# Optimization experiments

Hardware: AMD Instinct MI355X
Metric: run time of the kernel (lower is better)

## Reference

```python
import jax, jax.numpy as jnp
import numpy as np

N_HEADS = 16

def rotate_half(x):
    x1, x2 = jnp.split(x, 2, axis=-1)
    return jnp.concatenate([-x2, x1], axis=-1)

def setup_inputs() -> dict:
    key = jax.random.key(0)
    ks = jax.random.split(key, 6)
    dim = 2048
    B, T = 4, 2048
    x = jax.random.normal(ks[0], (B, T, dim), dtype=jnp.float32)
    pos = jnp.arange(T, dtype=jnp.float32).reshape(T, 1, 1)
    def w(k):
        return jax.random.normal(k, (dim, dim), dtype=jnp.float32) * 0.02
    return {
        "x": x, "pos": pos,
        "wq_w": w(ks[1]), "wq_b": jnp.zeros((dim,), jnp.float32),
        "wk_w": w(ks[2]), "wk_b": jnp.zeros((dim,), jnp.float32),
        "wv_w": w(ks[3]), "wv_b": jnp.zeros((dim,), jnp.float32),
        "wo_w": w(ks[4]), "wo_b": jnp.zeros((dim,), jnp.float32),
    }

def reference(x, pos, wq_w, wq_b, wk_w, wk_b, wv_w, wv_b, wo_w, wo_b):
    B, T, dim = x.shape
    H = N_HEADS
    hd = dim // H
    q = (x @ wq_w.T + wq_b).reshape(B, T, H, hd)
    k = (x @ wk_w.T + wk_b).reshape(B, T, H, hd)
    v = (x @ wv_w.T + wv_b).reshape(B, T, H, hd)
    # RoPE: freq over half the head dim, sin/cos tiled to full head dim
    freq = 1.0 / (10000.0 ** (jnp.arange(0, hd, 2, dtype=jnp.float32) / hd))  # [hd/2]
    ang = pos * freq                      # [T,1,hd/2]
    sin = jnp.concatenate([jnp.sin(ang), jnp.sin(ang)], axis=-1)  # [T,1,hd]
    cos = jnp.concatenate([jnp.cos(ang), jnp.cos(ang)], axis=-1)  # [T,1,hd]
    q = q * cos + rotate_half(q) * sin
    k = k * cos + rotate_half(k) * sin
    # [B,H,T,hd]
    q = q.transpose(0, 2, 1, 3)
    k = k.transpose(0, 2, 1, 3)
    v = v.transpose(0, 2, 1, 3)
    scale = 1.0 / np.sqrt(hd).astype(np.float32)
    attn = jnp.einsum('bhqd,bhkd->bhqk', q, k) * scale  # [B,H,T,T]
    attn = jax.nn.softmax(attn, axis=-1)
    out = jnp.einsum('bhqk,bhkd->bhqd', attn, v)        # [B,H,T,hd]
    out = out.transpose(0, 2, 1, 3).reshape(B, T, dim)
    return out @ wo_w.T + wo_b
```

## Files before the change

### kernel.cpp

```cpp
#include <hip/hip_runtime.h>


using floatx4  = __attribute__((ext_vector_type(4))) float;
using short8   = __attribute__((ext_vector_type(8))) short;
using ushortx4 = __attribute__((ext_vector_type(4))) unsigned short;

#define DEVFN static __device__ __forceinline__

DEVFN unsigned short f2bf(float f) {
  unsigned u = __builtin_bit_cast(unsigned, f);
  u += 0x7fffu + ((u >> 16) & 1u);
  return (unsigned short)(u >> 16);
}
DEVFN float bf2f(unsigned short h) {
  return __builtin_bit_cast(float, ((unsigned)h) << 16);
}

DEVFN void async_cp16(const unsigned short* g, unsigned short* l) {
  __builtin_amdgcn_global_load_lds(
      (const __attribute__((address_space(1))) void*)g,
      (__attribute__((address_space(3))) void*)l,
      16, 0, 0);
}

__global__ __launch_bounds__(256) void cast_kernel(const float4* __restrict__ in,
                                                   ushortx4* __restrict__ out) {
  long u = (long)blockIdx.x * 256 + threadIdx.x;
  float4 v = in[u];
  out[u] = (ushortx4){f2bf(v.x), f2bf(v.y), f2bf(v.z), f2bf(v.w)};
}

__global__ __launch_bounds__(256) void rope_kernel(unsigned short* __restrict__ Q,
                                                   unsigned short* __restrict__ K,
                                                   const float* __restrict__ pos) {
  long idx = (long)blockIdx.x * 256 + threadIdx.x;
  unsigned short* arr = (idx >> 23) ? K : Q;
  long rem = idx & ((1L << 23) - 1);
  long row = rem >> 6;
  int j = (int)(rem & 63);
  int t = (int)(row & 2047);
  float ang = pos[t] * exp2f(-0.20762051f * (float)j);
  float s = sinf(ang), c = cosf(ang);
  unsigned short* base = arr + (row << 7);
  float x1 = bf2f(base[j]), x2 = bf2f(base[j + 64]);
  base[j]      = f2bf(x1 * c - x2 * s);
  base[j + 64] = f2bf(x2 * c + x1 * s);
}

template <int MODE>
__global__ __launch_bounds__(256) void gemm_bt(const unsigned short* __restrict__ A,
                                               const unsigned short* __restrict__ Bw,
                                               const float* __restrict__ bias,
                                               void* __restrict__ Cout) {
  constexpr int K = 2048;
  __shared__ __align__(16) unsigned short lds_a[128 * 64];
  __shared__ __align__(16) unsigned short lds_b[128 * 64];
  const int tid = threadIdx.x;
  const int wave = tid >> 6, lane = tid & 63;
  const int ln15 = lane & 15, quad = lane >> 4;
  const int wr = wave >> 1, wc = wave & 1;
  const int bid = blockIdx.x;
  const int xcd = bid & 7, sl = bid >> 3;
  const int m0 = (xcd * 8 + (sl & 7)) * 128;
  const int n0 = (sl >> 3) * 128;

  floatx4 acc[4][4];
#pragma unroll
  for (int i = 0; i < 4; ++i)
#pragma unroll
    for (int j = 0; j < 4; ++j) acc[i][j] = (floatx4){0.f, 0.f, 0.f, 0.f};

  for (int k0 = 0; k0 < K; k0 += 64) {
    __syncthreads();
#pragma unroll
    for (int j = 0; j < 4; ++j) {
      int u = j * 256 + tid;
      int row = u >> 3;
      int c = (u & 7) ^ (row & 7);
      async_cp16(A + (long)(m0 + row) * K + (k0 + c * 8),
                 lds_a + (j * 256 + wave * 64) * 8);
    }
#pragma unroll
    for (int j = 0; j < 4; ++j) {
      int u = j * 256 + tid;
      int row = u >> 3;
      int c = (u & 7) ^ (row & 7);
      async_cp16(Bw + (long)(n0 + row) * K + (k0 + c * 8),
                 lds_b + (j * 256 + wave * 64) * 8);
    }
    asm volatile("s_waitcnt vmcnt(0)" ::: "memory");
    __syncthreads();
#pragma unroll
    for (int ks = 0; ks < 2; ++ks) {
      short8 af[4], bf[4];
#pragma unroll
      for (int mi = 0; mi < 4; ++mi) {
        int row = wr * 64 + mi * 16 + ln15;
        int phys = (ks * 4 + quad) ^ (row & 7);
        af[mi] = *(const short8*)(lds_a + row * 64 + phys * 8);
      }
#pragma unroll
      for (int ni = 0; ni < 4; ++ni) {
        int row = wc * 64 + ni * 16 + ln15;
        int phys = (ks * 4 + quad) ^ (row & 7);
        bf[ni] = *(const short8*)(lds_b + row * 64 + phys * 8);
      }
#pragma unroll
      for (int mi = 0; mi < 4; ++mi)
#pragma unroll
        for (int ni = 0; ni < 4; ++ni)
          acc[mi][ni] = __builtin_amdgcn_mfma_f32_16x16x32_bf16(af[mi], bf[ni],
                                                                acc[mi][ni], 0, 0, 0);
    }
  }

#pragma unroll
  for (int mi = 0; mi < 4; ++mi) {
#pragma unroll
    for (int ni = 0; ni < 4; ++ni) {
      int n = n0 + wc * 64 + ni * 16 + ln15;
      float bv = bias[n];
      int mbase = m0 + wr * 64 + mi * 16 + quad * 4;
      if (MODE == 0) {
        int h = n >> 7, d = n & 127;
#pragma unroll
        for (int r = 0; r < 4; ++r) {
          int m = mbase + r;
          int b = m >> 11, t = m & 2047;
          ((unsigned short*)Cout)[((((long)(b * 16 + h)) << 11) + t) * 128 + d] =
              f2bf(acc[mi][ni][r] + bv);
        }
      } else if (MODE == 1) {
        int h = n >> 7, d = n & 127;
        int b = mbase >> 11, t = mbase & 2047;
        ushortx4 v;
#pragma unroll
        for (int r = 0; r < 4; ++r) v[r] = f2bf(acc[mi][ni][r] + bv);
        *(ushortx4*)((unsigned short*)Cout +
                     ((((long)(b * 16 + h)) << 7) + d) * 2048 + t) = v;
      } else {
#pragma unroll
        for (int r = 0; r < 4; ++r) {
          int m = mbase + r;
          ((float*)Cout)[(long)m * 2048 + n] = acc[mi][ni][r] + bv;
        }
      }
    }
  }
}

__global__ __launch_bounds__(512, 2) void flash_kernel(
    const unsigned short* __restrict__ Q,
    const unsigned short* __restrict__ Kmat,
    const unsigned short* __restrict__ Vt,
    unsigned short* __restrict__ Out) {
  constexpr int T = 2048;
  constexpr float SCALE = 0.08838834764831845f;
  __shared__ __align__(16) unsigned short lds[49152];

  const int tid = threadIdx.x;
  const int wave = tid >> 6, lane = tid & 63;
  const int ln15 = lane & 15, quad = lane >> 4;
  const int l7 = ln15 & 7;
  const int bid = blockIdx.x;
  const int xcd = bid & 7, sl = bid >> 3;
  const int bh = xcd * 8 + (sl >> 3);
  const int q0 = (sl & 7) * 256;

  const unsigned short* Qb = Q + (long)bh * T * 128;
  const unsigned short* Kb = Kmat + (long)bh * T * 128;
  const unsigned short* Vb = Vt + (long)bh * 128 * T;
  unsigned short* pw = lds + 32768 + wave * 2048;

  short8 qf[2][4];
#pragma unroll
  for (int mi = 0; mi < 2; ++mi)
#pragma unroll
    for (int ks = 0; ks < 4; ++ks)
      qf[mi][ks] = *(const short8*)(Qb + (long)(q0 + wave * 32 + mi * 16 + ln15) * 128 +
                                    ks * 32 + quad * 8);

#define STAGE_KV(t, kdst, vdst)                                                  \
  do {                                                                           \
    _Pragma("unroll") for (int j = 0; j < 2; ++j) {                              \
      int u = j * 512 + tid;                                                     \
      int row = u >> 4;                                                          \
      int c = (u & 15) ^ (row & 15);                                             \
      async_cp16(Kb + (long)((t) * 64 + row) * 128 + c * 8,                      \
                 (kdst) + (j * 512 + wave * 64) * 8);                            \
    }                                                                            \
    _Pragma("unroll") for (int j = 0; j < 2; ++j) {                              \
      int u = j * 512 + tid;                                                     \
      int row = u >> 3;                                                          \
      int c = (u & 7) ^ (row & 7);                                               \
      async_cp16(Vb + (long)row * T + (t) * 64 + c * 8,                          \
                 (vdst) + (j * 512 + wave * 64) * 8);                            \
    }                                                                            \
  } while (0)

  STAGE_KV(0, lds, lds + 16384);
  asm volatile("s_waitcnt vmcnt(0)" ::: "memory");
  __syncthreads();

  floatx4 oacc[2][8];
#pragma unroll
  for (int mi = 0; mi < 2; ++mi)
#pragma unroll
    for (int nj = 0; nj < 8; ++nj) oacc[mi][nj] = (floatx4){0.f, 0.f, 0.f, 0.f};
  float mst[2][4], lsp[2][4];
#pragma unroll
  for (int mi = 0; mi < 2; ++mi)
#pragma unroll
    for (int r = 0; r < 4; ++r) { mst[mi][r] = -1e30f; lsp[mi][r] = 0.f; }

  for (int t = 0; t < 32; ++t) {
    unsigned short* kc = lds + (t & 1) * 8192;
    unsigned short* vc = lds + 16384 + (t & 1) * 8192;
    if (t < 31) {
      unsigned short* kn = lds + ((t + 1) & 1) * 8192;
      unsigned short* vn = lds + 16384 + ((t + 1) & 1) * 8192;
      STAGE_KV(t + 1, kn, vn);
    }

    floatx4 sacc[2][4];
#pragma unroll
    for (int mi = 0; mi < 2; ++mi)
#pragma unroll
      for (int ni = 0; ni < 4; ++ni) sacc[mi][ni] = (floatx4){0.f, 0.f, 0.f, 0.f};
#pragma unroll
    for (int ks = 0; ks < 4; ++ks) {
      short8 bfr[4];
#pragma unroll
      for (int ni = 0; ni < 4; ++ni) {
        int row = ni * 16 + ln15;
        int phys = (ks * 4 + quad) ^ ln15;
        bfr[ni] = *(const short8*)(kc + row * 128 + phys * 8);
      }
      __builtin_amdgcn_s_setprio(1);
#pragma unroll
      for (int mi = 0; mi < 2; ++mi)
#pragma unroll
        for (int ni = 0; ni < 4; ++ni)
          sacc[mi][ni] = __builtin_amdgcn_mfma_f32_16x16x32_bf16(qf[mi][ks], bfr[ni],
                                                                 sacc[mi][ni], 0, 0, 0);
      __builtin_amdgcn_s_setprio(0);
    }

#pragma unroll
    for (int mi = 0; mi < 2; ++mi)
#pragma unroll
      for (int r = 0; r < 4; ++r) {
        float mx = fmaxf(fmaxf(sacc[mi][0][r], sacc[mi][1][r]),
                         fmaxf(sacc[mi][2][r], sacc[mi][3][r]));
#pragma unroll
        for (int off = 1; off < 16; off <<= 1) mx = fmaxf(mx, __shfl_xor(mx, off, 16));
        mx *= SCALE;
        float mold = mst[mi][r];
        float mnew = fmaxf(mold, mx);
        float alpha = __expf(mold - mnew);
        float rs = 0.f;
#pragma unroll
        for (int ni = 0; ni < 4; ++ni) {
          float p = __expf(sacc[mi][ni][r] * SCALE - mnew);
          sacc[mi][ni][r] = p;
          rs += p;
        }
        mst[mi][r] = mnew;
        lsp[mi][r] = lsp[mi][r] * alpha + rs;
#pragma unroll
        for (int nj = 0; nj < 8; ++nj) oacc[mi][nj][r] *= alpha;
      }

#pragma unroll
    for (int mi = 0; mi < 2; ++mi)
#pragma unroll
      for (int ni = 0; ni < 4; ++ni) {
        int cc = ni * 2 + (ln15 >> 3);
#pragma unroll
        for (int r = 0; r < 4; ++r) {
          int m = mi * 16 + quad * 4 + r;
          pw[m * 64 + (cc ^ (m & 7)) * 8 + l7] = f2bf(sacc[mi][ni][r]);
        }
      }

#pragma unroll
    for (int ks = 0; ks < 2; ++ks) {
      short8 af[2], bv[8];
#pragma unroll
      for (int mi = 0; mi < 2; ++mi) {
        int phys = (ks * 4 + quad) ^ l7;
        af[mi] = *(const short8*)(pw + (mi * 16 + ln15) * 64 + phys * 8);
      }
#pragma unroll
      for (int nj = 0; nj < 8; ++nj) {
        int row = nj * 16 + ln15;
        int phys = (ks * 4 + quad) ^ (row & 7);
        bv[nj] = *(const short8*)(vc + row * 64 + phys * 8);
      }
      __builtin_amdgcn_s_setprio(1);
#pragma unroll
      for (int mi = 0; mi < 2; ++mi)
#pragma unroll
        for (int nj = 0; nj < 8; ++nj)
          oacc[mi][nj] = __builtin_amdgcn_mfma_f32_16x16x32_bf16(af[mi], bv[nj],
                                                                 oacc[mi][nj], 0, 0, 0);
      __builtin_amdgcn_s_setprio(0);
    }

    asm volatile("s_waitcnt vmcnt(0)" ::: "memory");
    __syncthreads();
  }
#undef STAGE_KV

  float rinv[2][4];
#pragma unroll
  for (int mi = 0; mi < 2; ++mi)
#pragma unroll
    for (int r = 0; r < 4; ++r) {
      float l = lsp[mi][r];
#pragma unroll
      for (int off = 1; off < 16; off <<= 1) l += __shfl_xor(l, off, 16);
      rinv[mi][r] = 1.f / l;
    }
#pragma unroll
  for (int mi = 0; mi < 2; ++mi)
#pragma unroll
    for (int nj = 0; nj < 8; ++nj)
#pragma unroll
      for (int r = 0; r < 4; ++r)
        lds[(wave * 32 + mi * 16 + quad * 4 + r) * 128 + nj * 16 + ln15] =
            f2bf(oacc[mi][nj][r] * rinv[mi][r]);
  __syncthreads();
  const int b = bh >> 4, h = bh & 15;
  long obase = ((long)(b * T + q0) << 11) + h * 128;
#pragma unroll
  for (int j = 0; j < 8; ++j) {
    int u = j * 512 + tid;
    int r = u >> 4, c = u & 15;
    *(short8*)(Out + obase + ((long)r << 11) + c * 8) =
        *(const short8*)(lds + r * 128 + c * 8);
  }
}

extern "C" void kernel_launch(void* const* d_in, const int* in_sizes, int n_in,
                              void* d_out, int out_size, void* d_ws, size_t ws_size,
                              hipStream_t stream) {
  const float* x    = (const float*)d_in[0];
  const float* pos  = (const float*)d_in[1];
  const float* wq_w = (const float*)d_in[2];
  const float* wq_b = (const float*)d_in[3];
  const float* wk_w = (const float*)d_in[4];
  const float* wk_b = (const float*)d_in[5];
  const float* wv_w = (const float*)d_in[6];
  const float* wv_b = (const float*)d_in[7];
  const float* wo_w = (const float*)d_in[8];
  const float* wo_b = (const float*)d_in[9];

  unsigned short* xb  = (unsigned short*)d_ws;
  unsigned short* wqb = xb  + (1u << 24);
  unsigned short* wkb = wqb + (1u << 22);
  unsigned short* wvb = wkb + (1u << 22);
  unsigned short* wob = wvb + (1u << 22);
  unsigned short* qb  = wob + (1u << 22);
  unsigned short* kb  = qb  + (1u << 24);
  unsigned short* vtb = kb  + (1u << 24);
  unsigned short* ab  = vtb + (1u << 24);

  cast_kernel<<<16384, 256, 0, stream>>>((const float4*)x, (ushortx4*)xb);
  cast_kernel<<<4096, 256, 0, stream>>>((const float4*)wq_w, (ushortx4*)wqb);
  cast_kernel<<<4096, 256, 0, stream>>>((const float4*)wk_w, (ushortx4*)wkb);
  cast_kernel<<<4096, 256, 0, stream>>>((const float4*)wv_w, (ushortx4*)wvb);
  cast_kernel<<<4096, 256, 0, stream>>>((const float4*)wo_w, (ushortx4*)wob);

  gemm_bt<0><<<1024, 256, 0, stream>>>(xb, wqb, wq_b, (void*)qb);
  gemm_bt<0><<<1024, 256, 0, stream>>>(xb, wkb, wk_b, (void*)kb);
  gemm_bt<1><<<1024, 256, 0, stream>>>(xb, wvb, wv_b, (void*)vtb);
  rope_kernel<<<65536, 256, 0, stream>>>(qb, kb, pos);
  flash_kernel<<<512, 512, 0, stream>>>(qb, kb, vtb, ab);
  gemm_bt<2><<<1024, 256, 0, stream>>>(ab, wob, wo_b, d_out);
}
```

Before: 748.4 us.

## Rewrite projection GEMM with 256x256 tiles, triple-buffered async loads, LDS-staged epilogue

Rewrites the projection GEMM to use 256x256 block tiles with 8 waves and a K-step of 32. Global-to-LDS copies are triple-buffered so loads for step t+2 overlap MFMA work on step t, replacing the load-wait-compute loop with a barrier every iteration. Output is staged through swizzled LDS so global stores become 16-byte coalesced writes, including the transposed V layout. The trade-off is more registers for the 8x4 accumulators and only 256 blocks, which may leave some CUs idle on a 256-CU part.

```diff
diff --git a/kernel.cpp b/kernel.cpp
--- a/kernel.cpp
+++ b/kernel.cpp
@@ -48,102 +48,208 @@
 }
 
 template <int MODE>
-__global__ __launch_bounds__(256) void gemm_bt(const unsigned short* __restrict__ A,
-                                               const unsigned short* __restrict__ Bw,
-                                               const float* __restrict__ bias,
-                                               void* __restrict__ Cout) {
+__global__ __launch_bounds__(512, 2) void gemm_bt(const unsigned short* __restrict__ A,
+                                                  const unsigned short* __restrict__ Bw,
+                                                  const float* __restrict__ bias,
+                                                  void* __restrict__ Cout) {
   constexpr int K = 2048;
-  __shared__ __align__(16) unsigned short lds_a[128 * 64];
-  __shared__ __align__(16) unsigned short lds_b[128 * 64];
+  constexpr int NT = 64;
+  __shared__ __align__(16) unsigned short lds[49152];
   const int tid = threadIdx.x;
   const int wave = tid >> 6, lane = tid & 63;
   const int ln15 = lane & 15, quad = lane >> 4;
-  const int wr = wave >> 1, wc = wave & 1;
+  const int wm = wave >> 2, wn = wave & 3;
   const int bid = blockIdx.x;
   const int xcd = bid & 7, sl = bid >> 3;
-  const int m0 = (xcd * 8 + (sl & 7)) * 128;
-  const int n0 = (sl >> 3) * 128;
-
-  floatx4 acc[4][4];
-#pragma unroll
-  for (int i = 0; i < 4; ++i)
+  const int m0 = (xcd * 4 + (sl & 3)) * 256;
+  const int n0 = (sl >> 2) * 256;
+
+  const unsigned short* srcA0;
+  const unsigned short* srcA1;
+  const unsigned short* srcB0;
+  const unsigned short* srcB1;
+  {
+    int u = tid;
+    int L = u >> 3, cc = (u & 7) ^ (L & 7);
+    int row = L * 2 + (cc >> 2), col = (cc & 3) * 8;
+    srcA0 = A + (long)(m0 + row) * K + col;
+    srcB0 = Bw + (long)(n0 + row) * K + col;
+  }
+  {
+    int u = tid + 512;
+    int L = u >> 3, cc = (u & 7) ^ (L & 7);
+    int row = L * 2 + (cc >> 2), col = (cc & 3) * 8;
+    srcA1 = A + (long)(m0 + row) * K + col;
+    srcB1 = Bw + (long)(n0 + row) * K + col;
+  }
+  const int sdst = wave * 512;
+
+#define STAGE_G(t, bufp)                                                \
+  do {                                                                  \
+    async_cp16(srcA0 + (long)(t) * 32, (bufp) + sdst);                  \
+    async_cp16(srcA1 + (long)(t) * 32, (bufp) + 4096 + sdst);           \
+    async_cp16(srcB0 + (long)(t) * 32, (bufp) + 8192 + sdst);           \
+    async_cp16(srcB1 + (long)(t) * 32, (bufp) + 12288 + sdst);          \
+  } while (0)
+
+  int offA[8], offB[4];
+#pragma unroll
+  for (int mi = 0; mi < 8; ++mi) {
+    int row = wm * 128 + mi * 16 + ln15;
+    int line = row >> 1, cc = (row & 1) * 4 + quad;
+    offA[mi] = line * 64 + (cc ^ (line & 7)) * 8;
+  }
+#pragma unroll
+  for (int nj = 0; nj < 4; ++nj) {
+    int row = wn * 64 + nj * 16 + ln15;
+    int line = row >> 1, cc = (row & 1) * 4 + quad;
+    offB[nj] = 8192 + line * 64 + (cc ^ (line & 7)) * 8;
+  }
+
+  floatx4 acc[8][4];
+#pragma unroll
+  for (int i = 0; i < 8; ++i)
 #pragma unroll
     for (int j = 0; j < 4; ++j) acc[i][j] = (floatx4){0.f, 0.f, 0.f, 0.f};
 
-  for (int k0 = 0; k0 < K; k0 += 64) {
-    __syncthreads();
-#pragma unroll
-    for (int j = 0; j < 4; ++j) {
-      int u = j * 256 + tid;
-      int row = u >> 3;
-      int c = (u & 7) ^ (row & 7);
-      async_cp16(A + (long)(m0 + row) * K + (k0 + c * 8),
-                 lds_a + (j * 256 + wave * 64) * 8);
-    }
-#pragma unroll
-    for (int j = 0; j < 4; ++j) {
-      int u = j * 256 + tid;
-      int row = u >> 3;
-      int c = (u & 7) ^ (row & 7);
-      async_cp16(Bw + (long)(n0 + row) * K + (k0 + c * 8),
-                 lds_b + (j * 256 + wave * 64) * 8);
-    }
-    asm volatile("s_waitcnt vmcnt(0)" ::: "memory");
-    __syncthreads();
-#pragma unroll
-    for (int ks = 0; ks < 2; ++ks) {
-      short8 af[4], bf[4];
-#pragma unroll
-      for (int mi = 0; mi < 4; ++mi) {
-        int row = wr * 64 + mi * 16 + ln15;
-        int phys = (ks * 4 + quad) ^ (row & 7);
-        af[mi] = *(const short8*)(lds_a + row * 64 + phys * 8);
-      }
-#pragma unroll
-      for (int ni = 0; ni < 4; ++ni) {
-        int row = wc * 64 + ni * 16 + ln15;
-        int phys = (ks * 4 + quad) ^ (row & 7);
-        bf[ni] = *(const short8*)(lds_b + row * 64 + phys * 8);
-      }
-#pragma unroll
-      for (int mi = 0; mi < 4; ++mi)
-#pragma unroll
-        for (int ni = 0; ni < 4; ++ni)
-          acc[mi][ni] = __builtin_amdgcn_mfma_f32_16x16x32_bf16(af[mi], bf[ni],
-                                                                acc[mi][ni], 0, 0, 0);
-    }
-  }
-
-#pragma unroll
-  for (int mi = 0; mi < 4; ++mi) {
-#pragma unroll
-    for (int ni = 0; ni < 4; ++ni) {
-      int n = n0 + wc * 64 + ni * 16 + ln15;
-      float bv = bias[n];
-      int mbase = m0 + wr * 64 + mi * 16 + quad * 4;
-      if (MODE == 0) {
-        int h = n >> 7, d = n & 127;
-#pragma unroll
-        for (int r = 0; r < 4; ++r) {
-          int m = mbase + r;
-          int b = m >> 11, t = m & 2047;
-          ((unsigned short*)Cout)[((((long)(b * 16 + h)) << 11) + t) * 128 + d] =
-              f2bf(acc[mi][ni][r] + bv);
+  unsigned short* const bA0 = lds;
+  unsigned short* const bA1 = lds + 16384;
+  unsigned short* const bA2 = lds + 32768;
+
+  STAGE_G(0, bA0);
+  STAGE_G(1, bA1);
+  asm volatile("s_waitcnt vmcnt(4)" ::: "memory");
+  __builtin_amdgcn_s_barrier();
+
+  int cb = 0;
+  for (int t = 0; t < NT; ++t) {
+    unsigned short* cur = (cb == 0) ? bA0 : ((cb == 1) ? bA1 : bA2);
+    if (t < NT - 2) {
+      int nb = cb ? cb - 1 : 2;
+      unsigned short* nxt = (nb == 0) ? bA0 : ((nb == 1) ? bA1 : bA2);
+      STAGE_G(t + 2, nxt);
+    }
+    short8 af[8], bf4[4];
+#pragma unroll
+    for (int mi = 0; mi < 8; ++mi) af[mi] = *(const short8*)(cur + offA[mi]);
+#pragma unroll
+    for (int nj = 0; nj < 4; ++nj) bf4[nj] = *(const short8*)(cur + offB[nj]);
+    __builtin_amdgcn_s_setprio(1);
+#pragma unroll
+    for (int mi = 0; mi < 8; ++mi)
+#pragma unroll
+      for (int nj = 0; nj < 4; ++nj)
+        acc[mi][nj] = __builtin_amdgcn_mfma_f32_16x16x32_bf16(af[mi], bf4[nj],
+                                                              acc[mi][nj], 0, 0, 0);
+    __builtin_amdgcn_s_setprio(0);
+    if (t < NT - 2) {
+      asm volatile("s_waitcnt vmcnt(4)" ::: "memory");
+    } else if (t == NT - 2) {
+      asm volatile("s_waitcnt vmcnt(0)" ::: "memory");
+    }
+    __builtin_amdgcn_s_barrier();
+    cb = (cb == 2) ? 0 : cb + 1;
+  }
+#undef STAGE_G
+
+  const int b_ = m0 >> 11;
+  const int t0m = m0 & 2047;
+  const int h0 = n0 >> 7;
+
+  if (MODE == 0) {
+#pragma unroll
+    for (int rnd = 0; rnd < 2; ++rnd) {
+      __syncthreads();
+      if (wm == rnd) {
+#pragma unroll
+        for (int nj = 0; nj < 4; ++nj) {
+          int nloc = wn * 64 + nj * 16 + ln15;
+          float bv = bias[n0 + nloc];
+#pragma unroll
+          for (int mi = 0; mi < 8; ++mi)
+#pragma unroll
+            for (int r = 0; r < 4; ++r) {
+              int tl = mi * 16 + quad * 4 + r;
+              int phys = (nloc >> 3) ^ (tl & 15);
+              lds[tl * 256 + phys * 8 + (nloc & 7)] = f2bf(acc[mi][nj][r] + bv);
+            }
         }
-      } else if (MODE == 1) {
-        int h = n >> 7, d = n & 127;
-        int b = mbase >> 11, t = mbase & 2047;
-        ushortx4 v;
-#pragma unroll
-        for (int r = 0; r < 4; ++r) v[r] = f2bf(acc[mi][ni][r] + bv);
-        *(ushortx4*)((unsigned short*)Cout +
-                     ((((long)(b * 16 + h)) << 7) + d) * 2048 + t) = v;
-      } else {
-#pragma unroll
-        for (int r = 0; r < 4; ++r) {
-          int m = mbase + r;
-          ((float*)Cout)[(long)m * 2048 + n] = acc[mi][ni][r] + bv;
+      }
+      __syncthreads();
+#pragma unroll
+      for (int j = 0; j < 8; ++j) {
+        int u = j * 512 + tid;
+        int tl = u >> 5, c = u & 31;
+        int phys = c ^ (tl & 15);
+        int h = h0 + (c >> 4);
+        int tt = t0m + rnd * 128 + tl;
+        *(short8*)((unsigned short*)Cout +
+                   ((((long)(b_ * 16 + h)) << 11) + tt) * 128 + (c & 15) * 8) =
+            *(const short8*)(lds + tl * 256 + phys * 8);
+      }
+    }
+  } else if (MODE == 1) {
+#pragma unroll
+    for (int rnd = 0; rnd < 2; ++rnd) {
+      __syncthreads();
+      if (wm == rnd) {
+#pragma unroll
+        for (int nj = 0; nj < 4; ++nj) {
+          int nloc = wn * 64 + nj * 16 + ln15;
+          float bv = bias[n0 + nloc];
+#pragma unroll
+          for (int mi = 0; mi < 8; ++mi)
+#pragma unroll
+            for (int r = 0; r < 4; ++r) {
+              int tl = mi * 16 + quad * 4 + r;
+              int phys = (tl >> 3) ^ (nloc & 15);
+              lds[nloc * 128 + phys * 8 + (tl & 7)] = f2bf(acc[mi][nj][r] + bv);
+            }
         }
+      }
+      __syncthreads();
+#pragma unroll
+      for (int j = 0; j < 8; ++j) {
+        int u = j * 512 + tid;
+        int nloc = u >> 4, c = u & 15;
+        int phys = c ^ (nloc & 15);
+        int h = h0 + (nloc >> 7), d = nloc & 127;
+        *(short8*)((unsigned short*)Cout +
+                   ((((long)(b_ * 16 + h)) << 7) + d) * 2048 + t0m + rnd * 128 + c * 8) =
+            *(const short8*)(lds + nloc * 128 + phys * 8);
+      }
+    }
+  } else {
+    float* lf = (float*)lds;
+#pragma unroll
+    for (int rnd = 0; rnd < 4; ++rnd) {
+      __syncthreads();
+      if (wm == (rnd >> 1)) {
+#pragma unroll
+        for (int nj = 0; nj < 4; ++nj) {
+          int nloc = wn * 64 + nj * 16 + ln15;
+          float bv = bias[n0 + nloc];
+#pragma unroll
+          for (int mh = 0; mh < 4; ++mh) {
+            int mi = (rnd & 1) * 4 + mh;
+#pragma unroll
+            for (int r = 0; r < 4; ++r) {
+              int tl = mh * 16 + quad * 4 + r;
+              int phys = (nloc >> 2) ^ (tl & 15);
+              lf[tl * 256 + phys * 4 + (nloc & 3)] = acc[mi][nj][r] + bv;
+            }
+          }
+        }
+      }
+      __syncthreads();
+#pragma unroll
+      for (int j = 0; j < 8; ++j) {
+        int u = j * 512 + tid;
+        int tl = u >> 6, c = u & 63;
+        int phys = c ^ (tl & 15);
+        int m = m0 + rnd * 64 + tl;
+        *(floatx4*)((float*)Cout + (long)m * 2048 + n0 + c * 4) =
+            *(const floatx4*)(lf + tl * 256 + phys * 4);
       }
     }
   }
@@ -372,10 +478,10 @@
   cast_kernel<<<4096, 256, 0, stream>>>((const float4*)wv_w, (ushortx4*)wvb);
   cast_kernel<<<4096, 256, 0, stream>>>((const float4*)wo_w, (ushortx4*)wob);
 
-  gemm_bt<0><<<1024, 256, 0, stream>>>(xb, wqb, wq_b, (void*)qb);
-  gemm_bt<0><<<1024, 256, 0, stream>>>(xb, wkb, wk_b, (void*)kb);
-  gemm_bt<1><<<1024, 256, 0, stream>>>(xb, wvb, wv_b, (void*)vtb);
+  gemm_bt<0><<<256, 512, 0, stream>>>(xb, wqb, wq_b, (void*)qb);
+  gemm_bt<0><<<256, 512, 0, stream>>>(xb, wkb, wk_b, (void*)kb);
+  gemm_bt<1><<<256, 512, 0, stream>>>(xb, wvb, wv_b, (void*)vtb);
   rope_kernel<<<65536, 256, 0, stream>>>(qb, kb, pos);
   flash_kernel<<<512, 512, 0, stream>>>(qb, kb, vtb, ab);
-  gemm_bt<2><<<1024, 256, 0, stream>>>(ab, wob, wo_b, d_out);
-}
+  gemm_bt<2><<<256, 512, 0, stream>>>(ab, wob, wo_b, d_out);
+}
```

Result: faster. 697.7 us (-6.8%).

## Fuse QKV GEMMs with RoPE epilogue and stage outputs through LDS for coalesced stores

Applied to the files above, without the earlier changes.

The three projection GEMMs become one launch of 3072 blocks, with the block index selecting Q, K or V weights. RoPE moves into the Q/K epilogue using a precomputed cos/sin table, which removes the separate read-modify-write rope pass over Q and K. All GEMM epilogues, including the output projection, now stage results through swizzled LDS so global stores are wide and coalesced instead of scattered scalar writes. The loops also hoist source pointers and raise wave priority around the MFMAs, at the cost of extra LDS traffic and barriers in the epilogue.

```diff
diff --git a/kernel.cpp b/kernel.cpp
--- a/kernel.cpp
+++ b/kernel.cpp
@@ -30,39 +30,57 @@
   out[u] = (ushortx4){f2bf(v.x), f2bf(v.y), f2bf(v.z), f2bf(v.w)};
 }
 
-__global__ __launch_bounds__(256) void rope_kernel(unsigned short* __restrict__ Q,
-                                                   unsigned short* __restrict__ K,
-                                                   const float* __restrict__ pos) {
-  long idx = (long)blockIdx.x * 256 + threadIdx.x;
-  unsigned short* arr = (idx >> 23) ? K : Q;
-  long rem = idx & ((1L << 23) - 1);
-  long row = rem >> 6;
-  int j = (int)(rem & 63);
-  int t = (int)(row & 2047);
+__global__ __launch_bounds__(256) void cs_table_kernel(const float* __restrict__ pos,
+                                                       float2* __restrict__ cst) {
+  int idx = blockIdx.x * 256 + threadIdx.x;
+  int t = idx >> 6, j = idx & 63;
   float ang = pos[t] * exp2f(-0.20762051f * (float)j);
-  float s = sinf(ang), c = cosf(ang);
-  unsigned short* base = arr + (row << 7);
-  float x1 = bf2f(base[j]), x2 = bf2f(base[j + 64]);
-  base[j]      = f2bf(x1 * c - x2 * s);
-  base[j + 64] = f2bf(x2 * c + x1 * s);
-}
-
-template <int MODE>
-__global__ __launch_bounds__(256) void gemm_bt(const unsigned short* __restrict__ A,
-                                               const unsigned short* __restrict__ Bw,
-                                               const float* __restrict__ bias,
-                                               void* __restrict__ Cout) {
+  cst[idx] = make_float2(cosf(ang), sinf(ang));
+}
+
+__global__ __launch_bounds__(256) void qkv_gemm(
+    const unsigned short* __restrict__ A,
+    const unsigned short* __restrict__ Wq, const unsigned short* __restrict__ Wk,
+    const unsigned short* __restrict__ Wv,
+    const float* __restrict__ bq, const float* __restrict__ bk,
+    const float* __restrict__ bv,
+    unsigned short* __restrict__ Oq, unsigned short* __restrict__ Ok,
+    unsigned short* __restrict__ Ov,
+    const float2* __restrict__ cst) {
   constexpr int K = 2048;
-  __shared__ __align__(16) unsigned short lds_a[128 * 64];
-  __shared__ __align__(16) unsigned short lds_b[128 * 64];
+  constexpr int NT = 32;
+  __shared__ __align__(16) unsigned short lds[16384];
   const int tid = threadIdx.x;
   const int wave = tid >> 6, lane = tid & 63;
   const int ln15 = lane & 15, quad = lane >> 4;
   const int wr = wave >> 1, wc = wave & 1;
   const int bid = blockIdx.x;
-  const int xcd = bid & 7, sl = bid >> 3;
-  const int m0 = (xcd * 8 + (sl & 7)) * 128;
-  const int n0 = (sl >> 3) * 128;
+  const int g = bid >> 10;
+  const int b2 = bid & 1023;
+  const unsigned short* Bw = (g == 0) ? Wq : (g == 1) ? Wk : Wv;
+  const float* bias = (g == 0) ? bq : (g == 1) ? bk : bv;
+  unsigned short* Cout = (g == 0) ? Oq : (g == 1) ? Ok : Ov;
+  const int xcd = b2 & 7, s = b2 >> 3;
+  const int m0 = (xcd * 8 + (s & 7)) * 128;
+  const int n0 = (s >> 3) * 128;
+
+  const unsigned short *sA0, *sA1, *sA2, *sA3, *sB0, *sB1, *sB2, *sB3;
+#define MKSRC(j, pa, pb)                                                \
+  {                                                                     \
+    int u = (j) * 256 + tid;                                            \
+    int L = u >> 3, c = (u & 7) ^ (L & 7);                              \
+    pa = A + (long)(m0 + L) * K + c * 8;                                \
+    pb = Bw + (long)(n0 + L) * K + c * 8;                               \
+  }
+  MKSRC(0, sA0, sB0) MKSRC(1, sA1, sB1) MKSRC(2, sA2, sB2) MKSRC(3, sA3, sB3)
+#undef MKSRC
+
+  int rowA[4], rowB[4];
+#pragma unroll
+  for (int i = 0; i < 4; ++i) {
+    rowA[i] = wr * 64 + i * 16 + ln15;
+    rowB[i] = wc * 64 + i * 16 + ln15;
+  }
 
   floatx4 acc[4][4];
 #pragma unroll
@@ -70,81 +88,211 @@
 #pragma unroll
     for (int j = 0; j < 4; ++j) acc[i][j] = (floatx4){0.f, 0.f, 0.f, 0.f};
 
-  for (int k0 = 0; k0 < K; k0 += 64) {
+  for (int t = 0; t < NT; ++t) {
     __syncthreads();
 #pragma unroll
     for (int j = 0; j < 4; ++j) {
+      const unsigned short* pa = (j == 0) ? sA0 : (j == 1) ? sA1 : (j == 2) ? sA2 : sA3;
+      const unsigned short* pb = (j == 0) ? sB0 : (j == 1) ? sB1 : (j == 2) ? sB2 : sB3;
+      async_cp16(pa + (long)t * 64, lds + (j * 256 + wave * 64) * 8);
+      async_cp16(pb + (long)t * 64, lds + 8192 + (j * 256 + wave * 64) * 8);
+    }
+    asm volatile("s_waitcnt vmcnt(0)" ::: "memory");
+    __syncthreads();
+#pragma unroll
+    for (int ks = 0; ks < 2; ++ks) {
+      short8 af[4], bf4[4];
+#pragma unroll
+      for (int mi = 0; mi < 4; ++mi) {
+        int phys = (ks * 4 + quad) ^ (rowA[mi] & 7);
+        af[mi] = *(const short8*)(lds + rowA[mi] * 64 + phys * 8);
+      }
+#pragma unroll
+      for (int nj = 0; nj < 4; ++nj) {
+        int phys = (ks * 4 + quad) ^ (rowB[nj] & 7);
+        bf4[nj] = *(const short8*)(lds + 8192 + rowB[nj] * 64 + phys * 8);
+      }
+      __builtin_amdgcn_s_setprio(1);
+#pragma unroll
+      for (int mi = 0; mi < 4; ++mi)
+#pragma unroll
+        for (int nj = 0; nj < 4; ++nj)
+          acc[mi][nj] = __builtin_amdgcn_mfma_f32_16x16x32_bf16(af[mi], bf4[nj],
+                                                                acc[mi][nj], 0, 0, 0);
+      __builtin_amdgcn_s_setprio(0);
+    }
+  }
+  __syncthreads();
+
+  const int b_ = m0 >> 11;
+  const int t0m = m0 & 2047;
+  const int h = n0 >> 7;
+
+  if (g == 2) {
+#pragma unroll
+    for (int nj = 0; nj < 4; ++nj) {
+      int nloc = wc * 64 + nj * 16 + ln15;
+      float bv = bias[n0 + nloc];
+#pragma unroll
+      for (int mi = 0; mi < 4; ++mi)
+#pragma unroll
+        for (int r = 0; r < 4; ++r) {
+          int tl = wr * 64 + mi * 16 + quad * 4 + r;
+          int phys = (tl >> 3) ^ (nloc & 15);
+          lds[nloc * 128 + phys * 8 + (tl & 7)] = f2bf(acc[mi][nj][r] + bv);
+        }
+    }
+    __syncthreads();
+#pragma unroll
+    for (int j = 0; j < 8; ++j) {
       int u = j * 256 + tid;
-      int row = u >> 3;
-      int c = (u & 7) ^ (row & 7);
-      async_cp16(A + (long)(m0 + row) * K + (k0 + c * 8),
-                 lds_a + (j * 256 + wave * 64) * 8);
-    }
+      int d = u >> 4, c = u & 15;
+      int phys = c ^ (d & 15);
+      *(short8*)(Cout + ((((long)(b_ * 16 + h)) << 7) + d) * 2048 + t0m + c * 8) =
+          *(const short8*)(lds + d * 128 + phys * 8);
+    }
+  } else {
+#pragma unroll
+    for (int nj = 0; nj < 4; ++nj) {
+      int nloc = wc * 64 + nj * 16 + ln15;
+      float bv = bias[n0 + nloc];
+#pragma unroll
+      for (int mi = 0; mi < 4; ++mi)
+#pragma unroll
+        for (int r = 0; r < 4; ++r) {
+          int tl = wr * 64 + mi * 16 + quad * 4 + r;
+          int phys = (nloc >> 3) ^ (tl & 15);
+          lds[tl * 128 + phys * 8 + (nloc & 7)] = f2bf(acc[mi][nj][r] + bv);
+        }
+    }
+    __syncthreads();
+#pragma unroll
+    for (int j = 0; j < 8; ++j) {
+      int u = j * 256 + tid;
+      int tl = u >> 4, c = u & 15;
+      int phys = c ^ (tl & 15);
+      int physp = (c ^ 8) ^ (tl & 15);
+      short8 s8 = *(const short8*)(lds + tl * 128 + phys * 8);
+      short8 p8 = *(const short8*)(lds + tl * 128 + physp * 8);
+      int tt = t0m + tl;
+      const float2* ct = cst + tt * 64 + (c & 7) * 8;
+      short8 o8;
+#pragma unroll
+      for (int e = 0; e < 8; ++e) {
+        float2 cs = ct[e];
+        float x = bf2f((unsigned short)s8[e]);
+        float y = bf2f((unsigned short)p8[e]);
+        float v = (c < 8) ? (x * cs.x - y * cs.y) : (x * cs.x + y * cs.y);
+        o8[e] = (short)f2bf(v);
+      }
+      *(short8*)(Cout + ((((long)(b_ * 16 + h)) << 11) + tt) * 128 + c * 8) = o8;
+    }
+  }
+}
+
+__global__ __launch_bounds__(256) void gemm_wo(const unsigned short* __restrict__ A,
+                                               const unsigned short* __restrict__ Bw,
+                                               const float* __restrict__ bias,
+                                               float* __restrict__ Cout) {
+  constexpr int K = 2048;
+  constexpr int NT = 32;
+  __shared__ __align__(16) unsigned short lds[16384];
+  const int tid = threadIdx.x;
+  const int wave = tid >> 6, lane = tid & 63;
+  const int ln15 = lane & 15, quad = lane >> 4;
+  const int wr = wave >> 1, wc = wave & 1;
+  const int bid = blockIdx.x;
+  const int xcd = bid & 7, s = bid >> 3;
+  const int m0 = (xcd * 8 + (s & 7)) * 128;
+  const int n0 = (s >> 3) * 128;
+
+  const unsigned short *sA0, *sA1, *sA2, *sA3, *sB0, *sB1, *sB2, *sB3;
+#define MKSRC(j, pa, pb)                                                \
+  {                                                                     \
+    int u = (j) * 256 + tid;                                            \
+    int L = u >> 3, c = (u & 7) ^ (L & 7);                              \
+    pa = A + (long)(m0 + L) * K + c * 8;                                \
+    pb = Bw + (long)(n0 + L) * K + c * 8;                               \
+  }
+  MKSRC(0, sA0, sB0) MKSRC(1, sA1, sB1) MKSRC(2, sA2, sB2) MKSRC(3, sA3, sB3)
+#undef MKSRC
+
+  int rowA[4], rowB[4];
+#pragma unroll
+  for (int i = 0; i < 4; ++i) {
+    rowA[i] = wr * 64 + i * 16 + ln15;
+    rowB[i] = wc * 64 + i * 16 + ln15;
+  }
+
+  floatx4 acc[4][4];
+#pragma unroll
+  for (int i = 0; i < 4; ++i)
+#pragma unroll
+    for (int j = 0; j < 4; ++j) acc[i][j] = (floatx4){0.f, 0.f, 0.f, 0.f};
+
+  for (int t = 0; t < NT; ++t) {
+    __syncthreads();
 #pragma unroll
     for (int j = 0; j < 4; ++j) {
+      const unsigned short* pa = (j == 0) ? sA0 : (j == 1) ? sA1 : (j == 2) ? sA2 : sA3;
+      const unsigned short* pb = (j == 0) ? sB0 : (j == 1) ? sB1 : (j == 2) ? sB2 : sB3;
+      async_cp16(pa + (long)t * 64, lds + (j * 256 + wave * 64) * 8);
+      async_cp16(pb + (long)t * 64, lds + 8192 + (j * 256 + wave * 64) * 8);
+    }
+    asm volatile("s_waitcnt vmcnt(0)" ::: "memory");
+    __syncthreads();
+#pragma unroll
+    for (int ks = 0; ks < 2; ++ks) {
+      short8 af[4], bf4[4];
+#pragma unroll
+      for (int mi = 0; mi < 4; ++mi) {
+        int phys = (ks * 4 + quad) ^ (rowA[mi] & 7);
+        af[mi] = *(const short8*)(lds + rowA[mi] * 64 + phys * 8);
+      }
+#pragma unroll
+      for (int nj = 0; nj < 4; ++nj) {
+        int phys = (ks * 4 + quad) ^ (rowB[nj] & 7);
+        bf4[nj] = *(const short8*)(lds + 8192 + rowB[nj] * 64 + phys * 8);
+      }
+      __builtin_amdgcn_s_setprio(1);
+#pragma unroll
+      for (int mi = 0; mi < 4; ++mi)
+#pragma unroll
+        for (int nj = 0; nj < 4; ++nj)
+          acc[mi][nj] = __builtin_amdgcn_mfma_f32_16x16x32_bf16(af[mi], bf4[nj],
+                                                                acc[mi][nj], 0, 0, 0);
+      __builtin_amdgcn_s_setprio(0);
+    }
+  }
+
+  float* lf = (float*)lds;
+#pragma unroll
+  for (int rnd = 0; rnd < 2; ++rnd) {
+    __syncthreads();
+    if (wr == rnd) {
+#pragma unroll
+      for (int nj = 0; nj < 4; ++nj) {
+        int nloc = wc * 64 + nj * 16 + ln15;
+        float bv = bias[n0 + nloc];
+#pragma unroll
+        for (int mi = 0; mi < 4; ++mi)
+#pragma unroll
+          for (int r = 0; r < 4; ++r) {
+            int tl = mi * 16 + quad * 4 + r;
+            int phys = (nloc >> 2) ^ (tl & 15);
+            lf[tl * 128 + phys * 4 + (nloc & 3)] = acc[mi][nj][r] + bv;
+          }
+      }
+    }
+    __syncthreads();
+#pragma unroll
+    for (int j = 0; j < 8; ++j) {
       int u = j * 256 + tid;
-      int row = u >> 3;
-      int c = (u & 7) ^ (row & 7);
-      async_cp16(Bw + (long)(n0 + row) * K + (k0 + c * 8),
-                 lds_b + (j * 256 + wave * 64) * 8);
-    }
-    asm volatile("s_waitcnt vmcnt(0)" ::: "memory");
-    __syncthreads();
-#pragma unroll
-    for (int ks = 0; ks < 2; ++ks) {
-      short8 af[4], bf[4];
-#pragma unroll
-      for (int mi = 0; mi < 4; ++mi) {
-        int row = wr * 64 + mi * 16 + ln15;
-        int phys = (ks * 4 + quad) ^ (row & 7);
-        af[mi] = *(const short8*)(lds_a + row * 64 + phys * 8);
-      }
-#pragma unroll
-      for (int ni = 0; ni < 4; ++ni) {
-        int row = wc * 64 + ni * 16 + ln15;
-        int phys = (ks * 4 + quad) ^ (row & 7);
-        bf[ni] = *(const short8*)(lds_b + row * 64 + phys * 8);
-      }
-#pragma unroll
-      for (int mi = 0; mi < 4; ++mi)
-#pragma unroll
-        for (int ni = 0; ni < 4; ++ni)
-          acc[mi][ni] = __builtin_amdgcn_mfma_f32_16x16x32_bf16(af[mi], bf[ni],
-                                                                acc[mi][ni], 0, 0, 0);
-    }
-  }
-
-#pragma unroll
-  for (int mi = 0; mi < 4; ++mi) {
-#pragma unroll
-    for (int ni = 0; ni < 4; ++ni) {
-      int n = n0 + wc * 64 + ni * 16 + ln15;
-      float bv = bias[n];
-      int mbase = m0 + wr * 64 + mi * 16 + quad * 4;
-      if (MODE == 0) {
-        int h = n >> 7, d = n & 127;
-#pragma unroll
-        for (int r = 0; r < 4; ++r) {
-          int m = mbase + r;
-          int b = m >> 11, t = m & 2047;
-          ((unsigned short*)Cout)[((((long)(b * 16 + h)) << 11) + t) * 128 + d] =
-              f2bf(acc[mi][ni][r] + bv);
-        }
-      } else if (MODE == 1) {
-        int h = n >> 7, d = n & 127;
-        int b = mbase >> 11, t = mbase & 2047;
-        ushortx4 v;
-#pragma unroll
-        for (int r = 0; r < 4; ++r) v[r] = f2bf(acc[mi][ni][r] + bv);
-        *(ushortx4*)((unsigned short*)Cout +
-                     ((((long)(b * 16 + h)) << 7) + d) * 2048 + t) = v;
-      } else {
-#pragma unroll
-        for (int r = 0; r < 4; ++r) {
-          int m = mbase + r;
-          ((float*)Cout)[(long)m * 2048 + n] = acc[mi][ni][r] + bv;
-        }
-      }
+      int tl = u >> 5, c = u & 31;
+      int phys = c ^ (tl & 15);
+      int m = m0 + rnd * 64 + tl;
+      *(floatx4*)(Cout + (long)m * 2048 + n0 + c * 4) =
+          *(const floatx4*)(lf + tl * 128 + phys * 4);
     }
   }
 }
@@ -365,17 +513,17 @@
   unsigned short* kb  = qb  + (1u << 24);
   unsigned short* vtb = kb  + (1u << 24);
   unsigned short* ab  = vtb + (1u << 24);
+  float2* cst = (float2*)ab;
 
   cast_kernel<<<16384, 256, 0, stream>>>((const float4*)x, (ushortx4*)xb);
   cast_kernel<<<4096, 256, 0, stream>>>((const float4*)wq_w, (ushortx4*)wqb);
   cast_kernel<<<4096, 256, 0, stream>>>((const float4*)wk_w, (ushortx4*)wkb);
   cast_kernel<<<4096, 256, 0, stream>>>((const float4*)wv_w, (ushortx4*)wvb);
   cast_kernel<<<4096, 256, 0, stream>>>((const float4*)wo_w, (ushortx4*)wob);
-
-  gemm_bt<0><<<1024, 256, 0, stream>>>(xb, wqb, wq_b, (void*)qb);
-  gemm_bt<0><<<1024, 256, 0, stream>>>(xb, wkb, wk_b, (void*)kb);
-  gemm_bt<1><<<1024, 256, 0, stream>>>(xb, wvb, wv_b, (void*)vtb);
-  rope_kernel<<<65536, 256, 0, stream>>>(qb, kb, pos);
+  cs_table_kernel<<<512, 256, 0, stream>>>(pos, cst);
+
+  qkv_gemm<<<3072, 256, 0, stream>>>(xb, wqb, wkb, wvb, wq_b, wk_b, wv_b,
+                                     qb, kb, vtb, cst);
   flash_kernel<<<512, 512, 0, stream>>>(qb, kb, vtb, ab);
-  gemm_bt<2><<<1024, 256, 0, stream>>>(ab, wob, wo_b, d_out);
-}
+  gemm_wo<<<1024, 256, 0, stream>>>(ab, wob, wo_b, (float*)d_out);
+}
```

Measured after the change: 720.4 us. 3.7% less time.
